# Kernel optimization log

Measured on AMD Instinct MI355X. Metric: run time of the kernel, lower is better.

Reference implementation:

```python
import jax, jax.numpy as jnp
import numpy as np

N_NODES = 100000
N_EDGES = 600000
HIDDEN = 128
LN_EPS = 1e-8


def setup_inputs() -> dict:
    key = jax.random.key(0)
    k1, k2, k3 = jax.random.split(key, 3)
    x = jax.random.normal(k1, (N_NODES, HIDDEN), dtype=jnp.float32)
    edge_index = jax.random.randint(k2, (2, N_EDGES), 0, N_NODES, dtype=jnp.int32)
    # GCNConv linear weight (glorot-ish scale) and bias
    W = jax.random.normal(k3, (HIDDEN, HIDDEN), dtype=jnp.float32) / np.sqrt(HIDDEN)
    b = jnp.zeros((HIDDEN,), dtype=jnp.float32)
    ln_gamma = jnp.ones((HIDDEN,), dtype=jnp.float32)
    ln_beta = jnp.zeros((HIDDEN,), dtype=jnp.float32)
    return {"x": x, "edge_index": edge_index, "W": W, "b": b,
            "ln_gamma": ln_gamma, "ln_beta": ln_beta}


def _gcn_layer(x, edge_index, W, b, ln_gamma, ln_beta):
    n = x.shape[0]
    # --- GCNConv (PyG semantics): add self-loops, sym-normalize, x@W, scatter ---
    loop = jnp.arange(n, dtype=edge_index.dtype)
    src = jnp.concatenate([edge_index[0], loop])  # [E+N]
    dst = jnp.concatenate([edge_index[1], loop])
    deg = jax.ops.segment_sum(jnp.ones_like(dst, dtype=x.dtype), dst,
                              num_segments=n)  # in-degree incl. self-loop
    dinv = jnp.where(deg > 0, jax.lax.rsqrt(deg), 0.0)
    norm = dinv[src] * dinv[dst]  # [E+N]
    h = x @ W  # [N, H]
    msg = h[src] * norm[:, None]  # gather + scale, [E+N, H]
    agg = jax.ops.segment_sum(msg, dst, num_segments=n) + b  # scatter-sum
    # --- ReLU -> (dropout = identity in eval) -> residual -> LayerNorm ---
    y = jax.nn.relu(agg) + x
    mu = jnp.mean(y, axis=-1, keepdims=True)
    var = jnp.mean(jnp.square(y - mu), axis=-1, keepdims=True)
    return (y - mu) * jax.lax.rsqrt(var + LN_EPS) * ln_gamma + ln_beta


def reference(x, edge_index, W, b, ln_gamma, ln_beta):
    return _gcn_layer(x, edge_index, W, b, ln_gamma, ln_beta)
```

## Files before the change

kernel.cpp:

```cpp
#include <hip/hip_runtime.h>

#define HID 128
#define CAP 32
#define BM 64

typedef unsigned short u16;
typedef unsigned int u32;
typedef __attribute__((ext_vector_type(8))) short short8v;
typedef __attribute__((ext_vector_type(4))) float f32x4;
typedef __attribute__((ext_vector_type(4))) u32 u32x4;

__device__ inline u16 f2bf(float f) {
    union { float f; u32 u; } c; c.f = f;
    u32 u = c.u;
    return (u16)((u + 0x7FFFu + ((u >> 16) & 1u)) >> 16);
}
__device__ inline u32 pack2(float lo, float hi) {
    return (u32)f2bf(lo) | ((u32)f2bf(hi) << 16);
}
__device__ inline float bflo(u32 u) {
    union { u32 u; float f; } c; c.u = u << 16; return c.f;
}
__device__ inline float bfhi(u32 u) {
    union { u32 u; float f; } c; c.u = u & 0xFFFF0000u; return c.f;
}

__global__ void k_countfill(const int* __restrict__ src, const int* __restrict__ dst,
                            int* __restrict__ cnt, int* __restrict__ csr, int e) {
    int i = blockIdx.x * blockDim.x + threadIdx.x;
    if (i < e) {
        int d = dst[i];
        int slot = atomicAdd(&cnt[d], 1);
        if (slot < CAP) csr[(size_t)d * CAP + slot] = src[i];
    }
}

__global__ __launch_bounds__(256) void k_prep(const float* __restrict__ x,
                                              u16* __restrict__ xbf,
                                              const int* __restrict__ cnt,
                                              float* __restrict__ dinv,
                                              const float* __restrict__ W,
                                              u16* __restrict__ wswz, int n) {
    int t = blockIdx.x * blockDim.x + threadIdx.x;
    if (t < n * 16) {
        int g = t >> 4, l = t & 15;
        const float4* p = (const float4*)&x[(size_t)g * HID + l * 8];
        float4 v0 = p[0], v1 = p[1];
        uint4 o;
        o.x = pack2(v0.x, v0.y);
        o.y = pack2(v0.z, v0.w);
        o.z = pack2(v1.x, v1.y);
        o.w = pack2(v1.z, v1.w);
        *(uint4*)&xbf[(size_t)g * HID + l * 8] = o;
    }
    if (t < n) dinv[t] = rsqrtf((float)(cnt[t] + 1));
    if (t < 128 * 128) {
        int i = t & 7;
        int lane = (t >> 3) & 63;
        int ct = (t >> 9) & 7;
        int ks = t >> 12;
        int k = ks * 32 + (lane >> 4) * 8 + i;
        int col = ct * 16 + (lane & 15);
        wswz[t] = f2bf(W[k * HID + col]);
    }
}

__global__ __launch_bounds__(256) void k_fused(const float* __restrict__ x,
                                               const u16* __restrict__ xbf,
                                               const float* __restrict__ dinv,
                                               const int* __restrict__ cnt,
                                               const int* __restrict__ csr,
                                               const u16* __restrict__ wswz,
                                               const float* __restrict__ bvec,
                                               const float* __restrict__ gamma,
                                               const float* __restrict__ beta,
                                               float* __restrict__ out, int n) {
    __shared__ uint4 lds4[1024];
    char* lds = (char*)lds4;
    const int tid = threadIdx.x;
    const int row0 = blockIdx.x * BM;

    {
        const int grp = tid >> 4;
        const int l16 = tid & 15;
        const int j8 = l16 * 8;
        #pragma unroll
        for (int k = 0; k < 4; ++k) {
            int r = grp * 4 + k;
            int g = row0 + r;
            uint4 pk = make_uint4(0, 0, 0, 0);
            if (g < n) {
                const float dd = dinv[g];
                float acc[8];
                {
                    float s2 = dd * dd;
                    u32x4 hv = *(const u32x4*)&xbf[(size_t)g * HID + j8];
                    acc[0] = bflo(hv.x) * s2; acc[1] = bfhi(hv.x) * s2;
                    acc[2] = bflo(hv.y) * s2; acc[3] = bfhi(hv.y) * s2;
                    acc[4] = bflo(hv.z) * s2; acc[5] = bfhi(hv.z) * s2;
                    acc[6] = bflo(hv.w) * s2; acc[7] = bfhi(hv.w) * s2;
                }
                const size_t off = (size_t)g * CAP;
                const int len = min(cnt[g], CAP);
                for (int base = 0; base < len; base += 16) {
                    int idx = base + l16;
                    int sk = csr[off + (idx < len ? idx : 0)];
                    float dv = (idx < len) ? dinv[sk] : 0.f;
                    int mm = (min(16, len - base) + 3) & ~3;
                    for (int j = 0; j < mm; j += 4) {
                        int s0 = __shfl(sk, j + 0, 16);
                        int s1 = __shfl(sk, j + 1, 16);
                        int s2 = __shfl(sk, j + 2, 16);
                        int s3 = __shfl(sk, j + 3, 16);
                        float w0 = __shfl(dv, j + 0, 16) * dd;
                        float w1 = __shfl(dv, j + 1, 16) * dd;
                        float w2 = __shfl(dv, j + 2, 16) * dd;
                        float w3 = __shfl(dv, j + 3, 16) * dd;
                        u32x4 h0 = *(const u32x4*)&xbf[(size_t)s0 * HID + j8];
                        u32x4 h1 = *(const u32x4*)&xbf[(size_t)s1 * HID + j8];
                        u32x4 h2 = *(const u32x4*)&xbf[(size_t)s2 * HID + j8];
                        u32x4 h3 = *(const u32x4*)&xbf[(size_t)s3 * HID + j8];
                        acc[0] = fmaf(bflo(h0.x), w0, acc[0]); acc[1] = fmaf(bfhi(h0.x), w0, acc[1]);
                        acc[2] = fmaf(bflo(h0.y), w0, acc[2]); acc[3] = fmaf(bfhi(h0.y), w0, acc[3]);
                        acc[4] = fmaf(bflo(h0.z), w0, acc[4]); acc[5] = fmaf(bfhi(h0.z), w0, acc[5]);
                        acc[6] = fmaf(bflo(h0.w), w0, acc[6]); acc[7] = fmaf(bfhi(h0.w), w0, acc[7]);
                        acc[0] = fmaf(bflo(h1.x), w1, acc[0]); acc[1] = fmaf(bfhi(h1.x), w1, acc[1]);
                        acc[2] = fmaf(bflo(h1.y), w1, acc[2]); acc[3] = fmaf(bfhi(h1.y), w1, acc[3]);
                        acc[4] = fmaf(bflo(h1.z), w1, acc[4]); acc[5] = fmaf(bfhi(h1.z), w1, acc[5]);
                        acc[6] = fmaf(bflo(h1.w), w1, acc[6]); acc[7] = fmaf(bfhi(h1.w), w1, acc[7]);
                        acc[0] = fmaf(bflo(h2.x), w2, acc[0]); acc[1] = fmaf(bfhi(h2.x), w2, acc[1]);
                        acc[2] = fmaf(bflo(h2.y), w2, acc[2]); acc[3] = fmaf(bfhi(h2.y), w2, acc[3]);
                        acc[4] = fmaf(bflo(h2.z), w2, acc[4]); acc[5] = fmaf(bfhi(h2.z), w2, acc[5]);
                        acc[6] = fmaf(bflo(h2.w), w2, acc[6]); acc[7] = fmaf(bfhi(h2.w), w2, acc[7]);
                        acc[0] = fmaf(bflo(h3.x), w3, acc[0]); acc[1] = fmaf(bfhi(h3.x), w3, acc[1]);
                        acc[2] = fmaf(bflo(h3.y), w3, acc[2]); acc[3] = fmaf(bfhi(h3.y), w3, acc[3]);
                        acc[4] = fmaf(bflo(h3.z), w3, acc[4]); acc[5] = fmaf(bfhi(h3.z), w3, acc[5]);
                        acc[6] = fmaf(bflo(h3.w), w3, acc[6]); acc[7] = fmaf(bfhi(h3.w), w3, acc[7]);
                    }
                }
                pk.x = pack2(acc[0], acc[1]);
                pk.y = pack2(acc[2], acc[3]);
                pk.z = pack2(acc[4], acc[5]);
                pk.w = pack2(acc[6], acc[7]);
            }
            int byte = r * 256 + l16 * 16;
            byte ^= (r & 7) << 4;
            *(uint4*)(lds + byte) = pk;
        }
    }
    __syncthreads();

    const int w = tid >> 6;
    const int l = tid & 63;
    const int c15 = l & 15;
    const short8v* wfrag = (const short8v*)wswz;

    f32x4 acc[8];
    #pragma unroll
    for (int c = 0; c < 8; ++c) acc[c] = (f32x4){0.f, 0.f, 0.f, 0.f};

    #pragma unroll
    for (int ks = 0; ks < 4; ++ks) {
        int row = w * 16 + c15;
        int byte = row * 256 + ks * 64 + (l >> 4) * 16;
        byte ^= (row & 7) << 4;
        short8v a = *(const short8v*)(lds + byte);
        #pragma unroll
        for (int ct = 0; ct < 8; ++ct) {
            short8v b = wfrag[(ks * 8 + ct) * 64 + l];
            acc[ct] = __builtin_amdgcn_mfma_f32_16x16x32_bf16(a, b, acc[ct], 0, 0, 0);
        }
    }

    float bb[8], gg[8], bz[8];
    #pragma unroll
    for (int ct = 0; ct < 8; ++ct) {
        bb[ct] = bvec[ct * 16 + c15];
        gg[ct] = gamma[ct * 16 + c15];
        bz[ct] = beta[ct * 16 + c15];
    }
    #pragma unroll
    for (int j = 0; j < 4; ++j) {
        int gr = row0 + w * 16 + (l >> 4) * 4 + j;
        if (gr < n) {
            const float* xr = x + (size_t)gr * HID + c15;
            float v[8];
            #pragma unroll
            for (int ct = 0; ct < 8; ++ct)
                v[ct] = fmaxf(acc[ct][j] + bb[ct], 0.f) + xr[ct * 16];
            float sum = 0.f;
            #pragma unroll
            for (int ct = 0; ct < 8; ++ct) sum += v[ct];
            #pragma unroll
            for (int o = 1; o < 16; o <<= 1) sum += __shfl_xor(sum, o, 16);
            float mu = sum * (1.0f / HID);
            float d[8], vs = 0.f;
            #pragma unroll
            for (int ct = 0; ct < 8; ++ct) { d[ct] = v[ct] - mu; vs = fmaf(d[ct], d[ct], vs); }
            #pragma unroll
            for (int o = 1; o < 16; o <<= 1) vs += __shfl_xor(vs, o, 16);
            float inv = rsqrtf(vs * (1.0f / HID) + 1e-8f);
            float* orow = out + (size_t)gr * HID + c15;
            #pragma unroll
            for (int ct = 0; ct < 8; ++ct)
                __builtin_nontemporal_store(fmaf(d[ct] * inv, gg[ct], bz[ct]), &orow[ct * 16]);
        }
    }
}

extern "C" void kernel_launch(void* const* d_in, const int* in_sizes, int n_in,
                              void* d_out, int out_size, void* d_ws, size_t ws_size,
                              hipStream_t stream) {
    const float* x     = (const float*)d_in[0];
    const int*   ei    = (const int*)d_in[1];
    const float* W     = (const float*)d_in[2];
    const float* b     = (const float*)d_in[3];
    const float* gamma = (const float*)d_in[4];
    const float* beta  = (const float*)d_in[5];
    float* out = (float*)d_out;

    const int n = in_sizes[0] / HID;
    const int e = in_sizes[1] / 2;
    const int* src = ei;
    const int* dst = ei + e;

    u16* xbf    = (u16*)d_ws;
    int* cnt    = (int*)(xbf + (size_t)n * HID);
    float* dinv = (float*)(cnt + n);
    int* csr    = (int*)(dinv + n);
    u16* wswz   = (u16*)(csr + (size_t)n * CAP);

    hipMemsetAsync(cnt, 0, (size_t)n * sizeof(int), stream);
    k_countfill<<<(e + 255) / 256, 256, 0, stream>>>(src, dst, cnt, csr, e);
    k_prep<<<((size_t)n * 16 + 255) / 256, 256, 0, stream>>>(x, xbf, cnt, dinv, W, wswz, n);

    k_fused<<<(n + BM - 1) / BM, 256, 0, stream>>>(
        x, xbf, dinv, cnt, csr, wswz, b, gamma, beta, out, n);
}
```

Baseline: 101.2 us.

## Merge CSR build into prep kernel, recompute dinv, use bf16 residual

Fuses the edge count/fill pass with the x-to-bf16 and weight swizzle pass into one kernel, removing a launch and a dependency. Drops the dinv array and recomputes rsqrt(deg) from counts in the aggregation kernel. Reads the residual from the bf16 copy of x instead of fp32 x to cut memory traffic, at the cost of residual precision. Uses nontemporal loads for CSR indices.

```diff
diff --git a/kernel.cpp b/kernel.cpp
--- a/kernel.cpp
+++ b/kernel.cpp
@@ -24,23 +24,18 @@
 __device__ inline float bfhi(u32 u) {
     union { u32 u; float f; } c; c.u = u & 0xFFFF0000u; return c.f;
 }
-
-__global__ void k_countfill(const int* __restrict__ src, const int* __restrict__ dst,
-                            int* __restrict__ cnt, int* __restrict__ csr, int e) {
-    int i = blockIdx.x * blockDim.x + threadIdx.x;
-    if (i < e) {
-        int d = dst[i];
-        int slot = atomicAdd(&cnt[d], 1);
-        if (slot < CAP) csr[(size_t)d * CAP + slot] = src[i];
-    }
-}
-
-__global__ __launch_bounds__(256) void k_prep(const float* __restrict__ x,
-                                              u16* __restrict__ xbf,
-                                              const int* __restrict__ cnt,
-                                              float* __restrict__ dinv,
-                                              const float* __restrict__ W,
-                                              u16* __restrict__ wswz, int n) {
+__device__ inline float bf2f(u16 b) {
+    union { u32 u; float f; } c; c.u = ((u32)b) << 16; return c.f;
+}
+
+__global__ __launch_bounds__(256) void k_build(const float* __restrict__ x,
+                                               u16* __restrict__ xbf,
+                                               const float* __restrict__ W,
+                                               u16* __restrict__ wswz,
+                                               const int* __restrict__ src,
+                                               const int* __restrict__ dst,
+                                               int* __restrict__ cnt,
+                                               int* __restrict__ csr, int n, int e) {
     int t = blockIdx.x * blockDim.x + threadIdx.x;
     if (t < n * 16) {
         int g = t >> 4, l = t & 15;
@@ -53,7 +48,11 @@
         o.w = pack2(v1.z, v1.w);
         *(uint4*)&xbf[(size_t)g * HID + l * 8] = o;
     }
-    if (t < n) dinv[t] = rsqrtf((float)(cnt[t] + 1));
+    if (t < e) {
+        int d = dst[t];
+        int slot = atomicAdd(&cnt[d], 1);
+        if (slot < CAP) csr[(size_t)d * CAP + slot] = src[t];
+    }
     if (t < 128 * 128) {
         int i = t & 7;
         int lane = (t >> 3) & 63;
@@ -65,9 +64,7 @@
     }
 }
 
-__global__ __launch_bounds__(256) void k_fused(const float* __restrict__ x,
-                                               const u16* __restrict__ xbf,
-                                               const float* __restrict__ dinv,
+__global__ __launch_bounds__(256) void k_fused(const u16* __restrict__ xbf,
                                                const int* __restrict__ cnt,
                                                const int* __restrict__ csr,
                                                const u16* __restrict__ wswz,
@@ -90,7 +87,8 @@
             int g = row0 + r;
             uint4 pk = make_uint4(0, 0, 0, 0);
             if (g < n) {
-                const float dd = dinv[g];
+                const int len = min(cnt[g], CAP);
+                const float dd = rsqrtf((float)(cnt[g] + 1));
                 float acc[8];
                 {
                     float s2 = dd * dd;
@@ -101,11 +99,10 @@
                     acc[6] = bflo(hv.w) * s2; acc[7] = bfhi(hv.w) * s2;
                 }
                 const size_t off = (size_t)g * CAP;
-                const int len = min(cnt[g], CAP);
                 for (int base = 0; base < len; base += 16) {
                     int idx = base + l16;
-                    int sk = csr[off + (idx < len ? idx : 0)];
-                    float dv = (idx < len) ? dinv[sk] : 0.f;
+                    int sk = __builtin_nontemporal_load(&csr[off + (idx < len ? idx : 0)]);
+                    float dv = (idx < len) ? rsqrtf((float)(cnt[sk] + 1)) : 0.f;
                     int mm = (min(16, len - base) + 3) & ~3;
                     for (int j = 0; j < mm; j += 4) {
                         int s0 = __shfl(sk, j + 0, 16);
@@ -183,11 +180,11 @@
     for (int j = 0; j < 4; ++j) {
         int gr = row0 + w * 16 + (l >> 4) * 4 + j;
         if (gr < n) {
-            const float* xr = x + (size_t)gr * HID + c15;
+            const u16* xr = xbf + (size_t)gr * HID + c15;
             float v[8];
             #pragma unroll
             for (int ct = 0; ct < 8; ++ct)
-                v[ct] = fmaxf(acc[ct][j] + bb[ct], 0.f) + xr[ct * 16];
+                v[ct] = fmaxf(acc[ct][j] + bb[ct], 0.f) + bf2f(xr[ct * 16]);
             float sum = 0.f;
             #pragma unroll
             for (int ct = 0; ct < 8; ++ct) sum += v[ct];
@@ -224,16 +221,14 @@
     const int* src = ei;
     const int* dst = ei + e;
 
-    u16* xbf    = (u16*)d_ws;
-    int* cnt    = (int*)(xbf + (size_t)n * HID);
-    float* dinv = (float*)(cnt + n);
-    int* csr    = (int*)(dinv + n);
-    u16* wswz   = (u16*)(csr + (size_t)n * CAP);
+    u16* xbf  = (u16*)d_ws;
+    int* cnt  = (int*)(xbf + (size_t)n * HID);
+    int* csr  = cnt + n;
+    u16* wswz = (u16*)(csr + (size_t)n * CAP);
 
     hipMemsetAsync(cnt, 0, (size_t)n * sizeof(int), stream);
-    k_countfill<<<(e + 255) / 256, 256, 0, stream>>>(src, dst, cnt, csr, e);
-    k_prep<<<((size_t)n * 16 + 255) / 256, 256, 0, stream>>>(x, xbf, cnt, dinv, W, wswz, n);
-
+    k_build<<<((size_t)n * 16 + 255) / 256, 256, 0, stream>>>(
+        x, xbf, W, wswz, src, dst, cnt, csr, n, e);
     k_fused<<<(n + BM - 1) / BM, 256, 0, stream>>>(
-        x, xbf, dinv, cnt, csr, wswz, b, gamma, beta, out, n);
-}
+        xbf, cnt, csr, wswz, b, gamma, beta, out, n);
+}
```

After: 97.98 us. 1.03x faster.
